# Performance work log

Measured on AMD Instinct MI355X. Metric: run time of the kernel, lower is better.

## Reference

```python
import jax, jax.numpy as jnp
import numpy as np

# Single LSTM cell step from ZERO initial state (h0=c0=0), vectorized over (B,T).
# PyTorch gate order: i, f, g, o. Since h0=0 the W_hh contribution is exactly 0
# and since c0=0 the forget-gate term vanishes: c = sigmoid(i)*tanh(g).

def _cell(inp, W_ih, b_ih, b_hh):
    # inp: (B,T,in), W_ih: (4H,in) -> gates (B,T,4H)
    g = jnp.einsum('bti,gi->btg', inp, W_ih) + b_ih + b_hh
    i_, f_, g_, o_ = jnp.split(g, 4, axis=-1)
    c = jax.nn.sigmoid(i_) * jnp.tanh(g_)
    h = jax.nn.sigmoid(o_) * jnp.tanh(c)
    return h, c


def setup_inputs() -> dict:
    key = jax.random.key(0)
    ks = jax.random.split(key, 11)
    B, T, E, H, V = 32, 256, 512, 512, 50000
    s = 1.0 / np.sqrt(H)  # keep gates out of deep saturation
    return {
        'x': jax.random.randint(ks[0], (B, T), 0, V, dtype=jnp.int32),
        'emb': jax.random.normal(ks[1], (V, E), jnp.float32),
        'W_ih_l0': jax.random.normal(ks[2], (2, 4 * H, E), jnp.float32) * s,
        'W_hh_l0': jax.random.normal(ks[3], (2, 4 * H, H), jnp.float32) * s,
        'b_ih_l0': jax.random.normal(ks[4], (2, 4 * H), jnp.float32) * s,
        'b_hh_l0': jax.random.normal(ks[5], (2, 4 * H), jnp.float32) * s,
        'W_ih_l1': jax.random.normal(ks[6], (2, 4 * H, 2 * H), jnp.float32) * s,
        'W_hh_l1': jax.random.normal(ks[7], (2, 4 * H, H), jnp.float32) * s,
        'b_ih_l1': jax.random.normal(ks[8], (2, 4 * H), jnp.float32) * s,
        'b_hh_l1': jax.random.normal(ks[9], (2, 4 * H), jnp.float32) * s,
    }


def reference(x, emb, W_ih_l0, W_hh_l0, b_ih_l0, b_hh_l0,
              W_ih_l1, W_hh_l1, b_ih_l1, b_hh_l1):
    e = emb[x]  # (B,T,E)
    # layer 0, forward/backward directions (seq_len==1 per step, so both
    # directions see the same token from zero state, with separate weights)
    h0f, c0f = _cell(e, W_ih_l0[0], b_ih_l0[0], b_hh_l0[0])
    h0b, c0b = _cell(e, W_ih_l0[1], b_ih_l0[1], b_hh_l0[1])
    inp1 = jnp.concatenate([h0f, h0b], axis=-1)  # (B,T,2H)
    h1f, c1f = _cell(inp1, W_ih_l1[0], b_ih_l1[0], b_hh_l1[0])
    h1b, c1b = _cell(inp1, W_ih_l1[1], b_ih_l1[1], b_hh_l1[1])
    # encoder_out: per-timestep h_n summed over directions -> (B,T,L,H)
    encoder_out = jnp.stack([h0f + h0b, h1f + h1b], axis=2)
    # h_last: forward-direction h_n and c_n at last timestep -> (L,B,H)
    h_last = jnp.stack([h0f[:, -1], h1f[:, -1]], axis=0)
    c_last = jnp.stack([c0f[:, -1], c1f[:, -1]], axis=0)
    return h_last, c_last, encoder_out
```

## Files before the change

### kernel.cpp

```cpp
#include <hip/hip_runtime.h>
#include <hip/hip_bf16.h>


using bf16x8 = __attribute__((ext_vector_type(8))) short;
using f32x4  = __attribute__((ext_vector_type(4))) float;

__device__ __forceinline__ float sigf(float x) { return 1.0f / (1.0f + expf(-x)); }
__device__ __forceinline__ unsigned short f2bf(float f)
{
    __hip_bfloat16 h = __float2bfloat16(f);
    return *(unsigned short*)&h;
}

__global__ void detect(const unsigned int* __restrict__ emb, int* __restrict__ flag)
{
    int ok = 0;
    for (int i = threadIdx.x; i < 256; i += 64) {
        unsigned lo = emb[i] & 0xFFFFu;
        int e = (lo >> 7) & 0xFF;
        if ((e >= 96 && e < 160) || lo == 0) ok++;
    }
#pragma unroll
    for (int off = 32; off; off >>= 1) ok += __shfl_down(ok, off);
    if (threadIdx.x == 0) *flag = (ok >= 192) ? 1 : 0;
}

__global__ void gather_convert(const int* __restrict__ x, const void* __restrict__ emb,
                               uint4* __restrict__ e0, const int* __restrict__ flag)
{
    int idx = blockIdx.x * 256 + threadIdx.x;
    int m = idx >> 6, r = idx & 63;
    long srow = x[m];
    uint4 v;
    if (*flag) {
        v = ((const uint4*)emb)[srow * 64 + r];
    } else {
        const float4* ef = (const float4*)emb;
        float4 a = ef[srow * 128 + r * 2], b = ef[srow * 128 + r * 2 + 1];
        unsigned short h[8] = { f2bf(a.x), f2bf(a.y), f2bf(a.z), f2bf(a.w),
                                f2bf(b.x), f2bf(b.y), f2bf(b.z), f2bf(b.w) };
        v = *(uint4*)h;
    }
    e0[idx] = v;
}

__global__ void pack_w(const void* __restrict__ src, uint4* __restrict__ dst,
                       int k8shift, const int* __restrict__ flag)
{
    int idx = blockIdx.x * 256 + threadIdx.x;
    int n = idx >> k8shift;
    int r = idx & ((1 << k8shift) - 1);
    int chunk = n >> 9;
    int dir = (chunk >= 3) ? 1 : 0;
    int gate = chunk - dir * 3;
    int sg = (gate == 0) ? 0 : (gate + 1);
    long srcrow = dir * 2048 + sg * 512 + (n & 511);
    long c8 = (srcrow << k8shift) + r;
    if (*flag) {
        dst[idx] = ((const uint4*)src)[c8];
    } else {
        const float4* sf = (const float4*)src;
        float4 a = sf[c8 * 2], b = sf[c8 * 2 + 1];
        unsigned short h[8] = { f2bf(a.x), f2bf(a.y), f2bf(a.z), f2bf(a.w),
                                f2bf(b.x), f2bf(b.y), f2bf(b.z), f2bf(b.w) };
        dst[idx] = *(uint4*)h;
    }
}

__global__ void pack_bias(const void* __restrict__ bi, const void* __restrict__ bh,
                          float* __restrict__ bc, const int* __restrict__ flag)
{
    int n = blockIdx.x * 256 + threadIdx.x;
    int chunk = n >> 9;
    int dir = (chunk >= 3) ? 1 : 0;
    int gate = chunk - dir * 3;
    int sg = (gate == 0) ? 0 : (gate + 1);
    int s = dir * 2048 + sg * 512 + (n & 511);
    float vi, vh;
    if (*flag) {
        vi = __bfloat162float(((const __hip_bfloat16*)bi)[s]);
        vh = __bfloat162float(((const __hip_bfloat16*)bh)[s]);
    } else {
        vi = ((const float*)bi)[s];
        vh = ((const float*)bh)[s];
    }
    bc[n] = vi + vh;
}

__global__ __launch_bounds__(256)
void gemm_gates(const unsigned short* __restrict__ A,
                const unsigned short* __restrict__ Bp,
                __hip_bfloat16* __restrict__ gates,
                int K)
{
    constexpr int BM = 128, BK = 32, NCOL = 3072;
    __shared__ __align__(16) unsigned short As[BM * BK];
    __shared__ __align__(16) unsigned short Bs[BM * BK];

    const int tid = threadIdx.x;
    const int bm = blockIdx.x;
    const int bn = blockIdx.y;
    const int K8 = K >> 3;

    const int ci0 = tid, ci1 = tid + 256;
    const int ar0 = ci0 >> 2, ar1 = ci1 >> 2;
    const uint4* a4 = (const uint4*)A;
    const uint4* b4 = (const uint4*)Bp;
    const long aBase0 = (long)(bm * BM + ar0) * K8 + (ci0 & 3);
    const long aBase1 = (long)(bm * BM + ar1) * K8 + (ci1 & 3);
    const long bBase0 = (long)(bn * BM + ar0) * K8 + (ci0 & 3);
    const long bBase1 = (long)(bn * BM + ar1) * K8 + (ci1 & 3);

    const int wave = tid >> 6, lane = tid & 63;
    const int wr = (wave >> 1) << 6;
    const int wc = (wave & 1) << 6;
    const int lr = lane & 15, q = lane >> 4;

    f32x4 acc[4][4] = {};

    for (int k0 = 0; k0 < K; k0 += BK) {
        const int k8 = k0 >> 3;
        uint4 va0 = a4[aBase0 + k8];
        uint4 va1 = a4[aBase1 + k8];
        uint4 vb0 = b4[bBase0 + k8];
        uint4 vb1 = b4[bBase1 + k8];

        __syncthreads();
        ((uint4*)As)[ci0] = va0;
        ((uint4*)As)[ci1] = va1;
        ((uint4*)Bs)[ci0] = vb0;
        ((uint4*)Bs)[ci1] = vb1;
        __syncthreads();

        bf16x8 af[4], bf[4];
#pragma unroll
        for (int i = 0; i < 4; ++i)
            af[i] = *(const bf16x8*)&As[(wr + i * 16 + lr) * BK + q * 8];
#pragma unroll
        for (int j = 0; j < 4; ++j)
            bf[j] = *(const bf16x8*)&Bs[(wc + j * 16 + lr) * BK + q * 8];
#pragma unroll
        for (int i = 0; i < 4; ++i)
#pragma unroll
            for (int j = 0; j < 4; ++j)
                acc[i][j] = __builtin_amdgcn_mfma_f32_16x16x32_bf16(af[i], bf[j], acc[i][j], 0, 0, 0);
    }

#pragma unroll
    for (int i = 0; i < 4; ++i) {
        long row = (long)bm * BM + wr + i * 16 + q * 4;
#pragma unroll
        for (int j = 0; j < 4; ++j) {
            int col = bn * BM + wc + j * 16 + lr;
#pragma unroll
            for (int r = 0; r < 4; ++r)
                gates[(row + r) * NCOL + col] = __float2bfloat16(acc[i][j][r]);
        }
    }
}

template <int LAYER>
__global__ void epilogue(const __hip_bfloat16* __restrict__ g,
                         const float* __restrict__ bc,
                         unsigned short* __restrict__ inp1,
                         void* __restrict__ outv,
                         const int* __restrict__ flag)
{
    int gid = blockIdx.x * 256 + threadIdx.x;
    int m = gid >> 9, h = gid & 511;
    long base = (long)m * 3072;
    float z[6];
#pragma unroll
    for (int d = 0; d < 2; ++d)
#pragma unroll
        for (int t = 0; t < 3; ++t) {
            int n = d * 1536 + t * 512 + h;
            z[d * 3 + t] = __bfloat162float(g[base + n]) + bc[n];
        }
    float c0 = sigf(z[0]) * tanhf(z[1]);
    float h0 = sigf(z[2]) * tanhf(c0);
    float c1 = sigf(z[3]) * tanhf(z[4]);
    float h1 = sigf(z[5]) * tanhf(c1);

    if constexpr (LAYER == 0) {
        inp1[(long)m * 1024 + h]       = f2bf(h0);
        inp1[(long)m * 1024 + 512 + h] = f2bf(h1);
    }

    const bool isbf = (*flag != 0);
    auto store = [&](long i, float v) {
        if (isbf) ((__hip_bfloat16*)outv)[i] = __float2bfloat16(v);
        else      ((float*)outv)[i] = v;
    };
    store(65536 + (long)m * 1024 + LAYER * 512 + h, h0 + h1);
    if ((m & 255) == 255) {
        int b = m >> 8;
        store(LAYER * 16384 + b * 512 + h, h0);
        store(32768 + LAYER * 16384 + b * 512 + h, c0);
    }
}

extern "C" void kernel_launch(void* const* d_in, const int* in_sizes, int n_in,
                              void* d_out, int out_size, void* d_ws, size_t ws_size,
                              hipStream_t stream)
{
    const int* x      = (const int*)d_in[0];
    const void* emb   = d_in[1];
    const void* Wih0  = d_in[2];
    const void* bih0  = d_in[4];
    const void* bhh0  = d_in[5];
    const void* Wih1  = d_in[6];
    const void* bih1  = d_in[8];
    const void* bhh1  = d_in[9];

    char* ws = (char*)d_ws;
    int*   flag           = (int*)(ws);
    float* bc0            = (float*)(ws + 1024);
    float* bc1            = (float*)(ws + 16384);
    unsigned short* Wp0   = (unsigned short*)(ws + 32768);
    unsigned short* Wp1   = (unsigned short*)(ws + 4194304);
    unsigned short* e0    = (unsigned short*)(ws + 10485760);
    unsigned short* inp1  = (unsigned short*)(ws + 18874368);
    __hip_bfloat16* gates = (__hip_bfloat16*)(ws + 35651584);

    detect<<<1, 64, 0, stream>>>((const unsigned int*)emb, flag);
    gather_convert<<<2048, 256, 0, stream>>>(x, emb, (uint4*)e0, flag);
    pack_w<<<768, 256, 0, stream>>>(Wih0, (uint4*)Wp0, 6, flag);
    pack_w<<<1536, 256, 0, stream>>>(Wih1, (uint4*)Wp1, 7, flag);
    pack_bias<<<12, 256, 0, stream>>>(bih0, bhh0, bc0, flag);
    pack_bias<<<12, 256, 0, stream>>>(bih1, bhh1, bc1, flag);

    gemm_gates<<<dim3(64, 24), 256, 0, stream>>>(e0, Wp0, gates, 512);
    epilogue<0><<<16384, 256, 0, stream>>>(gates, bc0, inp1, d_out, flag);

    gemm_gates<<<dim3(64, 24), 256, 0, stream>>>(inp1, Wp1, gates, 1024);
    epilogue<1><<<16384, 256, 0, stream>>>(gates, bc1, nullptr, d_out, flag);
}
```

Before: 336.9 us.

## Fuse LSTM gate epilogue into GEMM with interleaved weight packing and direct-to-LDS loads

The packed weight and bias layout changes so each hidden unit's six gate columns sit next to each other. The GEMM tile becomes 128x96, which lets each block compute complete gate sets and apply the sigmoid/tanh epilogue in-kernel through an LDS staging buffer. This removes the separate bf16 gates intermediate buffer and the two epilogue launches. Global loads now go straight to LDS via global_load_lds. The cost is narrower MFMA tiles (4x3), a two-pass epilogue with extra syncs, and no register double-buffering.

```diff
diff --git a/kernel.cpp b/kernel.cpp
--- a/kernel.cpp
+++ b/kernel.cpp
@@ -10,6 +10,13 @@
 {
     __hip_bfloat16 h = __float2bfloat16(f);
     return *(unsigned short*)&h;
+}
+
+__device__ __forceinline__ void gload16(const void* g, void* l)
+{
+    __builtin_amdgcn_global_load_lds(
+        (const __attribute__((address_space(1))) unsigned int*)g,
+        (__attribute__((address_space(3))) unsigned int*)l, 16, 0, 0);
 }
 
 __global__ void detect(const unsigned int* __restrict__ emb, int* __restrict__ flag)
@@ -50,20 +57,20 @@
     int idx = blockIdx.x * 256 + threadIdx.x;
     int n = idx >> k8shift;
     int r = idx & ((1 << k8shift) - 1);
-    int chunk = n >> 9;
-    int dir = (chunk >= 3) ? 1 : 0;
-    int gate = chunk - dir * 3;
+    int h = n / 6, gi = n % 6;
+    int dir = (gi >= 3) ? 1 : 0;
+    int gate = gi - dir * 3;
     int sg = (gate == 0) ? 0 : (gate + 1);
-    long srcrow = dir * 2048 + sg * 512 + (n & 511);
+    long srcrow = dir * 2048 + sg * 512 + h;
     long c8 = (srcrow << k8shift) + r;
     if (*flag) {
         dst[idx] = ((const uint4*)src)[c8];
     } else {
         const float4* sf = (const float4*)src;
         float4 a = sf[c8 * 2], b = sf[c8 * 2 + 1];
-        unsigned short h[8] = { f2bf(a.x), f2bf(a.y), f2bf(a.z), f2bf(a.w),
-                                f2bf(b.x), f2bf(b.y), f2bf(b.z), f2bf(b.w) };
-        dst[idx] = *(uint4*)h;
+        unsigned short h8[8] = { f2bf(a.x), f2bf(a.y), f2bf(a.z), f2bf(a.w),
+                                 f2bf(b.x), f2bf(b.y), f2bf(b.z), f2bf(b.w) };
+        dst[idx] = *(uint4*)h8;
     }
 }
 
@@ -71,11 +78,11 @@
                           float* __restrict__ bc, const int* __restrict__ flag)
 {
     int n = blockIdx.x * 256 + threadIdx.x;
-    int chunk = n >> 9;
-    int dir = (chunk >= 3) ? 1 : 0;
-    int gate = chunk - dir * 3;
+    int h = n / 6, gi = n % 6;
+    int dir = (gi >= 3) ? 1 : 0;
+    int gate = gi - dir * 3;
     int sg = (gate == 0) ? 0 : (gate + 1);
-    int s = dir * 2048 + sg * 512 + (n & 511);
+    int s = dir * 2048 + sg * 512 + h;
     float vi, vh;
     if (*flag) {
         vi = __bfloat162float(((const __hip_bfloat16*)bi)[s]);
@@ -87,104 +94,67 @@
     bc[n] = vi + vh;
 }
 
+template <int LAYER>
 __global__ __launch_bounds__(256)
-void gemm_gates(const unsigned short* __restrict__ A,
+void gemm_fused(const unsigned short* __restrict__ A,
                 const unsigned short* __restrict__ Bp,
-                __hip_bfloat16* __restrict__ gates,
+                const float* __restrict__ bc,
+                unsigned short* __restrict__ inp1,
+                void* __restrict__ outv,
+                const int* __restrict__ flag,
                 int K)
 {
-    constexpr int BM = 128, BK = 32, NCOL = 3072;
-    __shared__ __align__(16) unsigned short As[BM * BK];
-    __shared__ __align__(16) unsigned short Bs[BM * BK];
+    constexpr int BM = 128, BN = 96, BK = 32;
+    __shared__ __align__(16) char smem[64 * 97 * 4];
+    unsigned short* As = (unsigned short*)smem;
+    unsigned short* Bs = (unsigned short*)(smem + 8192);
+    float* Cs = (float*)smem;
 
     const int tid = threadIdx.x;
     const int bm = blockIdx.x;
     const int bn = blockIdx.y;
     const int K8 = K >> 3;
 
-    const int ci0 = tid, ci1 = tid + 256;
-    const int ar0 = ci0 >> 2, ar1 = ci1 >> 2;
     const uint4* a4 = (const uint4*)A;
     const uint4* b4 = (const uint4*)Bp;
-    const long aBase0 = (long)(bm * BM + ar0) * K8 + (ci0 & 3);
-    const long aBase1 = (long)(bm * BM + ar1) * K8 + (ci1 & 3);
-    const long bBase0 = (long)(bn * BM + ar0) * K8 + (ci0 & 3);
-    const long bBase1 = (long)(bn * BM + ar1) * K8 + (ci1 & 3);
+    uint4* As4 = (uint4*)As;
+    uint4* Bs4 = (uint4*)Bs;
+
+    const int ciA1 = tid + 256;
+    const int ciB1 = tid + 256;
+    const long aOff0 = (long)(bm * BM + (tid  >> 2)) * K8 + (tid  & 3);
+    const long aOff1 = (long)(bm * BM + (ciA1 >> 2)) * K8 + (ciA1 & 3);
+    const long bOff0 = (long)(bn * BN + (tid  >> 2)) * K8 + (tid  & 3);
+    const long bOff1 = (long)(bn * BN + (ciB1 >> 2)) * K8 + (ciB1 & 3);
 
     const int wave = tid >> 6, lane = tid & 63;
     const int wr = (wave >> 1) << 6;
-    const int wc = (wave & 1) << 6;
+    const int wc = (wave & 1) * 48;
     const int lr = lane & 15, q = lane >> 4;
 
-    f32x4 acc[4][4] = {};
+    f32x4 acc[4][3] = {};
 
     for (int k0 = 0; k0 < K; k0 += BK) {
         const int k8 = k0 >> 3;
-        uint4 va0 = a4[aBase0 + k8];
-        uint4 va1 = a4[aBase1 + k8];
-        uint4 vb0 = b4[bBase0 + k8];
-        uint4 vb1 = b4[bBase1 + k8];
-
-        __syncthreads();
-        ((uint4*)As)[ci0] = va0;
-        ((uint4*)As)[ci1] = va1;
-        ((uint4*)Bs)[ci0] = vb0;
-        ((uint4*)Bs)[ci1] = vb1;
-        __syncthreads();
-
-        bf16x8 af[4], bf[4];
+        __syncthreads();
+        gload16(a4 + aOff0 + k8, As4 + tid);
+        gload16(a4 + aOff1 + k8, As4 + ciA1);
+        gload16(b4 + bOff0 + k8, Bs4 + tid);
+        if (tid < 128) gload16(b4 + bOff1 + k8, Bs4 + ciB1);
+        __syncthreads();
+
+        bf16x8 af[4], bf[3];
 #pragma unroll
         for (int i = 0; i < 4; ++i)
             af[i] = *(const bf16x8*)&As[(wr + i * 16 + lr) * BK + q * 8];
 #pragma unroll
-        for (int j = 0; j < 4; ++j)
+        for (int j = 0; j < 3; ++j)
             bf[j] = *(const bf16x8*)&Bs[(wc + j * 16 + lr) * BK + q * 8];
 #pragma unroll
         for (int i = 0; i < 4; ++i)
 #pragma unroll
-            for (int j = 0; j < 4; ++j)
+            for (int j = 0; j < 3; ++j)
                 acc[i][j] = __builtin_amdgcn_mfma_f32_16x16x32_bf16(af[i], bf[j], acc[i][j], 0, 0, 0);
-    }
-
-#pragma unroll
-    for (int i = 0; i < 4; ++i) {
-        long row = (long)bm * BM + wr + i * 16 + q * 4;
-#pragma unroll
-        for (int j = 0; j < 4; ++j) {
-            int col = bn * BM + wc + j * 16 + lr;
-#pragma unroll
-            for (int r = 0; r < 4; ++r)
-                gates[(row + r) * NCOL + col] = __float2bfloat16(acc[i][j][r]);
-        }
-    }
-}
-
-template <int LAYER>
-__global__ void epilogue(const __hip_bfloat16* __restrict__ g,
-                         const float* __restrict__ bc,
-                         unsigned short* __restrict__ inp1,
-                         void* __restrict__ outv,
-                         const int* __restrict__ flag)
-{
-    int gid = blockIdx.x * 256 + threadIdx.x;
-    int m = gid >> 9, h = gid & 511;
-    long base = (long)m * 3072;
-    float z[6];
-#pragma unroll
-    for (int d = 0; d < 2; ++d)
-#pragma unroll
-        for (int t = 0; t < 3; ++t) {
-            int n = d * 1536 + t * 512 + h;
-            z[d * 3 + t] = __bfloat162float(g[base + n]) + bc[n];
-        }
-    float c0 = sigf(z[0]) * tanhf(z[1]);
-    float h0 = sigf(z[2]) * tanhf(c0);
-    float c1 = sigf(z[3]) * tanhf(z[4]);
-    float h1 = sigf(z[5]) * tanhf(c1);
-
-    if constexpr (LAYER == 0) {
-        inp1[(long)m * 1024 + h]       = f2bf(h0);
-        inp1[(long)m * 1024 + 512 + h] = f2bf(h1);
     }
 
     const bool isbf = (*flag != 0);
@@ -192,11 +162,50 @@
         if (isbf) ((__hip_bfloat16*)outv)[i] = __float2bfloat16(v);
         else      ((float*)outv)[i] = v;
     };
-    store(65536 + (long)m * 1024 + LAYER * 512 + h, h0 + h1);
-    if ((m & 255) == 255) {
-        int b = m >> 8;
-        store(LAYER * 16384 + b * 512 + h, h0);
-        store(32768 + LAYER * 16384 + b * 512 + h, c0);
+
+    const int hl = tid & 15;
+    float bcv[6];
+#pragma unroll
+    for (int gi = 0; gi < 6; ++gi) bcv[gi] = bc[bn * BN + hl * 6 + gi];
+
+#pragma unroll
+    for (int pass = 0; pass < 2; ++pass) {
+        __syncthreads();
+        if ((wr >> 6) == pass) {
+#pragma unroll
+            for (int i = 0; i < 4; ++i)
+#pragma unroll
+                for (int j = 0; j < 3; ++j)
+#pragma unroll
+                    for (int r = 0; r < 4; ++r)
+                        Cs[(i * 16 + q * 4 + r) * 97 + wc + j * 16 + lr] = acc[i][j][r];
+        }
+        __syncthreads();
+#pragma unroll
+        for (int t = 0; t < 4; ++t) {
+            int ml = (tid >> 4) + t * 16;
+            float z[6];
+#pragma unroll
+            for (int gi = 0; gi < 6; ++gi) z[gi] = Cs[ml * 97 + hl * 6 + gi] + bcv[gi];
+            float c0 = sigf(z[0]) * tanhf(z[1]);
+            float h0 = sigf(z[2]) * tanhf(c0);
+            float c1 = sigf(z[3]) * tanhf(z[4]);
+            float h1 = sigf(z[5]) * tanhf(c1);
+
+            long m = (long)bm * BM + pass * 64 + ml;
+            int hg = bn * 16 + hl;
+
+            if constexpr (LAYER == 0) {
+                inp1[m * 1024 + hg]       = f2bf(h0);
+                inp1[m * 1024 + 512 + hg] = f2bf(h1);
+            }
+            store(65536 + m * 1024 + LAYER * 512 + hg, h0 + h1);
+            if ((m & 255) == 255) {
+                int b = (int)(m >> 8);
+                store(LAYER * 16384 + b * 512 + hg, h0);
+                store(32768 + LAYER * 16384 + b * 512 + hg, c0);
+            }
+        }
     }
 }
 
@@ -221,7 +230,6 @@
     unsigned short* Wp1   = (unsigned short*)(ws + 4194304);
     unsigned short* e0    = (unsigned short*)(ws + 10485760);
     unsigned short* inp1  = (unsigned short*)(ws + 18874368);
-    __hip_bfloat16* gates = (__hip_bfloat16*)(ws + 35651584);
 
     detect<<<1, 64, 0, stream>>>((const unsigned int*)emb, flag);
     gather_convert<<<2048, 256, 0, stream>>>(x, emb, (uint4*)e0, flag);
@@ -230,9 +238,6 @@
     pack_bias<<<12, 256, 0, stream>>>(bih0, bhh0, bc0, flag);
     pack_bias<<<12, 256, 0, stream>>>(bih1, bhh1, bc1, flag);
 
-    gemm_gates<<<dim3(64, 24), 256, 0, stream>>>(e0, Wp0, gates, 512);
-    epilogue<0><<<16384, 256, 0, stream>>>(gates, bc0, inp1, d_out, flag);
-
-    gemm_gates<<<dim3(64, 24), 256, 0, stream>>>(inp1, Wp1, gates, 1024);
-    epilogue<1><<<16384, 256, 0, stream>>>(gates, bc1, nullptr, d_out, flag);
-}
+    gemm_fused<0><<<dim3(64, 32), 256, 0, stream>>>(e0, Wp0, bc0, inp1, d_out, flag, 512);
+    gemm_fused<1><<<dim3(64, 32), 256, 0, stream>>>(inp1, Wp1, bc1, nullptr, d_out, flag, 1024);
+}
```

Result: faster. 314.5 us (-6.6%).
